# Kernel tuning notes

Hardware: AMD Instinct MI355X
Metric: run time of the kernel (lower is better)

## Reference

```python
import jax, jax.numpy as jnp
import numpy as np

BATCH = 512
SEQ = 500          # number of time points; SEQ-1 spline pieces
INPUT_CH = 8       # input (control) channels
HIDDEN = 64        # hidden channels (size of z)
HH = 128           # hidden_hidden channels of the CDE func MLP
OUT = 1            # output channels


def setup_inputs() -> dict:
    key = jax.random.key(0)
    ks = jax.random.split(key, 12)
    shp = (BATCH, SEQ - 1, INPUT_CH)
    times = jnp.linspace(0.0, 1.0, SEQ, dtype=jnp.float32)
    coeff_a = jax.random.normal(ks[0], shp, dtype=jnp.float32)
    coeff_b = jax.random.normal(ks[1], shp, dtype=jnp.float32)
    coeff_two_c = jax.random.normal(ks[2], shp, dtype=jnp.float32)
    coeff_three_d = jax.random.normal(ks[3], shp, dtype=jnp.float32)
    # learned parameters
    init_W = jax.random.normal(ks[4], (INPUT_CH, HIDDEN), dtype=jnp.float32) / np.sqrt(INPUT_CH)
    init_b = jnp.zeros((HIDDEN,), dtype=jnp.float32)
    f_W1 = jax.random.normal(ks[5], (HIDDEN, HH), dtype=jnp.float32) / np.sqrt(HIDDEN)
    f_b1 = jnp.zeros((HH,), dtype=jnp.float32)
    f_W2 = jax.random.normal(ks[6], (HH, HIDDEN * INPUT_CH), dtype=jnp.float32) / np.sqrt(HH)
    f_b2 = jnp.zeros((HIDDEN * INPUT_CH,), dtype=jnp.float32)
    lin_W = jax.random.normal(ks[7], (HIDDEN, OUT), dtype=jnp.float32) / np.sqrt(HIDDEN)
    lin_b = jnp.zeros((OUT,), dtype=jnp.float32)
    return dict(times=times, coeff_a=coeff_a, coeff_b=coeff_b,
                coeff_two_c=coeff_two_c, coeff_three_d=coeff_three_d,
                init_W=init_W, init_b=init_b, f_W1=f_W1, f_b1=f_b1,
                f_W2=f_W2, f_b2=f_b2, lin_W=lin_W, lin_b=lin_b)


def reference(times, coeff_a, coeff_b, coeff_two_c, coeff_three_d,
              init_W, init_b, f_W1, f_b1, f_W2, f_b2, lin_W, lin_b):
    n_pieces = coeff_b.shape[1]

    def _interpret_t(t):
        idx = jnp.clip(jnp.sum(t > times) - 1, 0, n_pieces - 1)
        frac = t - times[idx]
        return frac, idx

    def spline_eval(t):  # NaturalCubicSpline.evaluate -> (B, INPUT_CH)
        frac, idx = _interpret_t(t)
        inner = 0.5 * coeff_two_c[:, idx] + coeff_three_d[:, idx] * frac / 3.0
        inner = coeff_b[:, idx] + inner * frac
        return coeff_a[:, idx] + inner * frac

    def dX_dt(t):  # NaturalCubicSpline.derivative -> (B, INPUT_CH)
        frac, idx = _interpret_t(t)
        inner = coeff_two_c[:, idx] + coeff_three_d[:, idx] * frac
        return coeff_b[:, idx] + inner * frac

    def f(z):  # CDE vector field MLP -> (B, HIDDEN, INPUT_CH)
        h = jax.nn.relu(z @ f_W1 + f_b1)
        v = jnp.tanh(h @ f_W2 + f_b2)
        return v.reshape(z.shape[0], HIDDEN, INPUT_CH)

    def F(t, z):  # VectorField: f(z) @ dX/dt -> (B, HIDDEN)
        return jnp.einsum('bhi,bi->bh', f(z), dX_dt(t))

    # initial state from initial_network applied to X(t0)
    z0 = spline_eval(times[0]) @ init_W + init_b  # (B, HIDDEN)

    @jax.checkpoint
    def rk4_step(z, i):
        t0 = times[i]
        h = times[i + 1] - times[i]
        k1 = F(t0, z)
        k2 = F(t0 + 0.5 * h, z + 0.5 * h * k1)
        k3 = F(t0 + 0.5 * h, z + 0.5 * h * k2)
        k4 = F(t0 + h, z + h * k3)
        z_next = z + (h / 6.0) * (k1 + 2.0 * k2 + 2.0 * k3 + k4)
        return z_next, None

    zT, _ = jax.lax.scan(rk4_step, z0, jnp.arange(SEQ - 1))
    # final linear readout + sigmoid activation
    return jax.nn.sigmoid(zT @ lin_W + lin_b)  # (B, OUT)
```

## Files before the change

### kernel.cpp

```cpp
#include <hip/hip_runtime.h>
#include <hip/hip_bf16.h>

#define NPIECE 499

typedef __attribute__((ext_vector_type(8))) short bf16x8;
typedef __attribute__((ext_vector_type(4))) short s16x4;
typedef __attribute__((ext_vector_type(4))) float f32x4;

__device__ inline short f2bf(float x) {
    union { float f; unsigned u; } v; v.f = x;
    unsigned r = v.u + 0x7FFFu + ((v.u >> 16) & 1u);
    return (short)(r >> 16);
}

__device__ inline float fast_tanh(float x) {
    float e = __expf(2.0f * x);
    return 1.0f - 2.0f * __builtin_amdgcn_rcpf(e + 1.0f);
}

__global__ void __launch_bounds__(512, 2)
cde_kernel(const float* __restrict__ times,
           const float* __restrict__ ca,  const float* __restrict__ cb,
           const float* __restrict__ c2c, const float* __restrict__ c3d,
           const float* __restrict__ initW, const float* __restrict__ initb,
           const float* __restrict__ W1,  const float* __restrict__ b1,
           const float* __restrict__ W2,  const float* __restrict__ b2,
           const float* __restrict__ linW, const float* __restrict__ linb,
           float* __restrict__ out)
{
    const int tid  = threadIdx.x;
    const int lane = tid & 63;
    const int wv   = tid >> 6;
    const int g    = lane >> 4;
    const int col  = lane & 15;
    const int s0   = blockIdx.x * 2;

    __shared__ __align__(16) short hbuf[4][64][8];
    __shared__ __align__(16) short zbuf[2][64][8];
    __shared__ __align__(16) float vbuf[2][512];
    __shared__ __align__(16) float zcur[2][64];
    __shared__ __align__(16) float dxbuf[2][3][2][8];

    bf16x8 a2[4][4];
    float  binit2[4][4];
#pragma unroll
    for (int ot = 0; ot < 4; ++ot) {
        int o = 64 * wv + 16 * ot + col;
#pragma unroll
        for (int kk = 0; kk < 4; ++kk) {
            bf16x8 f;
#pragma unroll
            for (int e = 0; e < 8; ++e)
                f[e] = f2bf(W2[(32 * kk + 8 * g + e) * 512 + o]);
            a2[ot][kk] = f;
        }
#pragma unroll
        for (int r = 0; r < 4; ++r)
            binit2[ot][r] = b2[64 * wv + 16 * ot + 4 * g + r];
    }
    bf16x8 a1[2];
#pragma unroll
    for (int kk = 0; kk < 2; ++kk) {
        bf16x8 f;
#pragma unroll
        for (int e = 0; e < 8; ++e)
            f[e] = f2bf(W1[(32 * kk + 8 * g + e) * 128 + 16 * wv + col]);
        a1[kk] = f;
    }
    float binit1[4];
#pragma unroll
    for (int r = 0; r < 4; ++r) binit1[r] = b1[16 * wv + 4 * g + r];

    if (tid < 128) {
        int s = tid >> 6, hid = tid & 63;
        float z = initb[hid];
#pragma unroll
        for (int c = 0; c < 8; ++c)
            z += ca[((s0 + s) * NPIECE + 0) * 8 + c] * initW[c * 64 + hid];
        zcur[s][hid] = z;
        int ksub = hid >> 5, kin = hid & 31;
        zbuf[ksub][((kin >> 3) << 4) | s][kin & 7] = f2bf(z);
    }
    __syncthreads();

    float zreg = 0.f, zsreg = 0.f;
    {
        int m = lane & 31, s = lane >> 5;
        if ((m & 3) == 0) zreg = zcur[s][8 * wv + (m >> 2)];
    }

    for (int i = 0; i < NPIECE; ++i) {
        const float t0 = times[i];
        const float t1 = times[i + 1];
        const float h  = t1 - t0;
        const int par  = i & 1;

        if (tid < 16) {
            int s = tid >> 3, c = tid & 7;
            int rowbase = (s0 + s) * NPIECE * 8;
            int p0 = (i > 0) ? i - 1 : 0;
            float f0 = t0 - times[p0];
            int b0 = rowbase + p0 * 8 + c;
            dxbuf[par][0][s][c] = cb[b0] + (c2c[b0] + c3d[b0] * f0) * f0;
            float th = t0 + 0.5f * h;
            float f1 = th - t0;
            int bi = rowbase + i * 8 + c;
            dxbuf[par][1][s][c] = cb[bi] + (c2c[bi] + c3d[bi] * f1) * f1;
            float t3 = t0 + h;
            int bx; float f2v;
            if (i < NPIECE - 1 && t3 > t1) { bx = rowbase + (i + 1) * 8 + c; f2v = t3 - t1; }
            else                            { bx = bi;                        f2v = t3 - t0; }
            dxbuf[par][2][s][c] = cb[bx] + (c2c[bx] + c3d[bx] * f2v) * f2v;
        }

#pragma unroll
        for (int st = 0; st < 4; ++st) {
            const int dsel = (st == 0) ? 0 : ((st == 3) ? 2 : 1);
            __syncthreads();

            bf16x8 bz0 = *(const bf16x8*)&zbuf[0][lane][0];
            bf16x8 bz1 = *(const bf16x8*)&zbuf[1][lane][0];
            f32x4 acc1 = {binit1[0], binit1[1], binit1[2], binit1[3]};
            acc1 = __builtin_amdgcn_mfma_f32_16x16x32_bf16(a1[0], bz0, acc1, 0, 0, 0);
            acc1 = __builtin_amdgcn_mfma_f32_16x16x32_bf16(a1[1], bz1, acc1, 0, 0, 0);
            if (col < 2) {
                int h0 = 16 * wv + 4 * g;
                int ksub = h0 >> 5, kin = h0 & 31;
                s16x4 t;
                t[0] = f2bf(fmaxf(acc1[0], 0.f));
                t[1] = f2bf(fmaxf(acc1[1], 0.f));
                t[2] = f2bf(fmaxf(acc1[2], 0.f));
                t[3] = f2bf(fmaxf(acc1[3], 0.f));
                *(s16x4*)&hbuf[ksub][((kin >> 3) << 4) | col][kin & 7] = t;
            }
            __syncthreads();

            bf16x8 bh0 = *(const bf16x8*)&hbuf[0][lane][0];
            bf16x8 bh1 = *(const bf16x8*)&hbuf[1][lane][0];
            bf16x8 bh2 = *(const bf16x8*)&hbuf[2][lane][0];
            bf16x8 bh3 = *(const bf16x8*)&hbuf[3][lane][0];
            f32x4 c0 = {binit2[0][0], binit2[0][1], binit2[0][2], binit2[0][3]};
            f32x4 c1 = {binit2[1][0], binit2[1][1], binit2[1][2], binit2[1][3]};
            f32x4 c2r = {binit2[2][0], binit2[2][1], binit2[2][2], binit2[2][3]};
            f32x4 c3r = {binit2[3][0], binit2[3][1], binit2[3][2], binit2[3][3]};
            c0  = __builtin_amdgcn_mfma_f32_16x16x32_bf16(a2[0][0], bh0, c0, 0, 0, 0);
            c1  = __builtin_amdgcn_mfma_f32_16x16x32_bf16(a2[1][0], bh0, c1, 0, 0, 0);
            c2r = __builtin_amdgcn_mfma_f32_16x16x32_bf16(a2[2][0], bh0, c2r, 0, 0, 0);
            c3r = __builtin_amdgcn_mfma_f32_16x16x32_bf16(a2[3][0], bh0, c3r, 0, 0, 0);
            c0  = __builtin_amdgcn_mfma_f32_16x16x32_bf16(a2[0][1], bh1, c0, 0, 0, 0);
            c1  = __builtin_amdgcn_mfma_f32_16x16x32_bf16(a2[1][1], bh1, c1, 0, 0, 0);
            c2r = __builtin_amdgcn_mfma_f32_16x16x32_bf16(a2[2][1], bh1, c2r, 0, 0, 0);
            c3r = __builtin_amdgcn_mfma_f32_16x16x32_bf16(a2[3][1], bh1, c3r, 0, 0, 0);
            c0  = __builtin_amdgcn_mfma_f32_16x16x32_bf16(a2[0][2], bh2, c0, 0, 0, 0);
            c1  = __builtin_amdgcn_mfma_f32_16x16x32_bf16(a2[1][2], bh2, c1, 0, 0, 0);
            c2r = __builtin_amdgcn_mfma_f32_16x16x32_bf16(a2[2][2], bh2, c2r, 0, 0, 0);
            c3r = __builtin_amdgcn_mfma_f32_16x16x32_bf16(a2[3][2], bh2, c3r, 0, 0, 0);
            c0  = __builtin_amdgcn_mfma_f32_16x16x32_bf16(a2[0][3], bh3, c0, 0, 0, 0);
            c1  = __builtin_amdgcn_mfma_f32_16x16x32_bf16(a2[1][3], bh3, c1, 0, 0, 0);
            c2r = __builtin_amdgcn_mfma_f32_16x16x32_bf16(a2[2][3], bh3, c2r, 0, 0, 0);
            c3r = __builtin_amdgcn_mfma_f32_16x16x32_bf16(a2[3][3], bh3, c3r, 0, 0, 0);

            if (col < 2) {
                *(f32x4*)&vbuf[col][64 * wv + 0  + 4 * g] = c0;
                *(f32x4*)&vbuf[col][64 * wv + 16 + 4 * g] = c1;
                *(f32x4*)&vbuf[col][64 * wv + 32 + 4 * g] = c2r;
                *(f32x4*)&vbuf[col][64 * wv + 48 + 4 * g] = c3r;
            }
            asm volatile("s_waitcnt lgkmcnt(0)" ::: "memory");
            __builtin_amdgcn_wave_barrier();

            {
                int m = lane & 31, s = lane >> 5;
                int o = 64 * wv + 2 * m;
                float2 vv = *(const float2*)&vbuf[s][o];
                float va = fast_tanh(vv.x);
                float vb = fast_tanh(vv.y);
                const float* dxp = &dxbuf[par][dsel][s][0];
                float d0 = dxp[(2 * m) & 7];
                float d1 = dxp[(2 * m + 1) & 7];
                float p = va * d0 + vb * d1;
                p += __shfl_xor(p, 1);
                p += __shfl_xor(p, 2);
                if ((m & 3) == 0) {
                    int hid = 8 * wv + (m >> 2);
                    float k = p;
                    float zst;
                    if (st == 0)      { zsreg = k;             zst = zreg + 0.5f * h * k; }
                    else if (st == 1) { zsreg += 2.f * k;      zst = zreg + 0.5f * h * k; }
                    else if (st == 2) { zsreg += 2.f * k;      zst = zreg + h * k; }
                    else              { zsreg += k;            zst = zreg + (h / 6.f) * zsreg;
                                        zreg = zst;            zcur[s][hid] = zst; }
                    int ksub = hid >> 5, kin = hid & 31;
                    zbuf[ksub][((kin >> 3) << 4) | s][kin & 7] = f2bf(zst);
                }
            }
        }
    }

    __syncthreads();
    if (tid < 2) {
        float acc = linb[0];
        for (int hd = 0; hd < 64; ++hd) acc += zcur[tid][hd] * linW[hd];
        out[s0 + tid] = 1.0f / (1.0f + __expf(-acc));
    }
}

extern "C" void kernel_launch(void* const* d_in, const int* in_sizes, int n_in,
                              void* d_out, int out_size, void* d_ws, size_t ws_size,
                              hipStream_t stream) {
    (void)in_sizes; (void)n_in; (void)d_ws; (void)ws_size; (void)out_size;
    const float* times = (const float*)d_in[0];
    const float* ca    = (const float*)d_in[1];
    const float* cb    = (const float*)d_in[2];
    const float* c2c   = (const float*)d_in[3];
    const float* c3d   = (const float*)d_in[4];
    const float* initW = (const float*)d_in[5];
    const float* initb = (const float*)d_in[6];
    const float* W1    = (const float*)d_in[7];
    const float* b1    = (const float*)d_in[8];
    const float* W2    = (const float*)d_in[9];
    const float* b2    = (const float*)d_in[10];
    const float* linW  = (const float*)d_in[11];
    const float* linb  = (const float*)d_in[12];
    cde_kernel<<<256, 512, 0, stream>>>(times, ca, cb, c2c, c3d, initW, initb,
                                        W1, b1, W2, b2, linW, linb, (float*)d_out);
}
```

Measured before the change: 1.808 ms.

## Process one sample per 256-thread block and prefetch spline derivatives ahead

Each block now handles a single batch sample with four waves instead of two samples with eight waves, so each wave holds twice as many W2 tiles in registers (8x4 bf16x8 fragments) and does twice the MFMA work per stage. The spline-derivative values for the next piece are loaded into registers early in the iteration and written to shared memory in the last stage, overlapping global latency with compute. Times and b2 are cached in shared memory, the bias is added after the MFMA, and the final readout uses a wave shuffle reduction. The risk is higher register pressure from the doubled weight fragments, and the MFMA B operand now carries only one useful column out of sixteen.

```diff
diff --git a/kernel.cpp b/kernel.cpp
--- a/kernel.cpp
+++ b/kernel.cpp
@@ -2,6 +2,7 @@
 #include <hip/hip_bf16.h>
 
 #define NPIECE 499
+#define SEQN 500
 
 typedef __attribute__((ext_vector_type(8))) short bf16x8;
 typedef __attribute__((ext_vector_type(4))) short s16x4;
@@ -18,7 +19,7 @@
     return 1.0f - 2.0f * __builtin_amdgcn_rcpf(e + 1.0f);
 }
 
-__global__ void __launch_bounds__(512, 2)
+__global__ void __launch_bounds__(256, 2)
 cde_kernel(const float* __restrict__ times,
            const float* __restrict__ ca,  const float* __restrict__ cb,
            const float* __restrict__ c2c, const float* __restrict__ c3d,
@@ -33,84 +34,96 @@
     const int wv   = tid >> 6;
     const int g    = lane >> 4;
     const int col  = lane & 15;
-    const int s0   = blockIdx.x * 2;
-
-    __shared__ __align__(16) short hbuf[4][64][8];
-    __shared__ __align__(16) short zbuf[2][64][8];
-    __shared__ __align__(16) float vbuf[2][512];
-    __shared__ __align__(16) float zcur[2][64];
-    __shared__ __align__(16) float dxbuf[2][3][2][8];
-
-    bf16x8 a2[4][4];
-    float  binit2[4][4];
-#pragma unroll
-    for (int ot = 0; ot < 4; ++ot) {
-        int o = 64 * wv + 16 * ot + col;
+    const int s    = blockIdx.x;
+
+    __shared__ __align__(16) float tl[SEQN];
+    __shared__ __align__(16) float b2l[512];
+    __shared__ __align__(16) float vbuf[4][128];
+    __shared__ __align__(16) short hflat[128];
+    __shared__ __align__(16) short zflat[64];
+    __shared__ __align__(16) float zcur[64];
+    __shared__ __align__(16) float dxb[2][3][8];
+
+    for (int j = tid; j < SEQN; j += 256) tl[j] = times[j];
+    for (int j = tid; j < 512; j += 256) b2l[j] = b2[j];
+
+    bf16x8 a2[8][4];
+#pragma unroll
+    for (int t = 0; t < 8; ++t) {
+        int o = 128 * wv + 16 * t + col;
 #pragma unroll
         for (int kk = 0; kk < 4; ++kk) {
             bf16x8 f;
 #pragma unroll
             for (int e = 0; e < 8; ++e)
                 f[e] = f2bf(W2[(32 * kk + 8 * g + e) * 512 + o]);
-            a2[ot][kk] = f;
+            a2[t][kk] = f;
+        }
+    }
+    bf16x8 a1[2][2];
+    float binit1[2][4];
+#pragma unroll
+    for (int t = 0; t < 2; ++t) {
+        int o = 32 * wv + 16 * t + col;
+#pragma unroll
+        for (int kk = 0; kk < 2; ++kk) {
+            bf16x8 f;
+#pragma unroll
+            for (int e = 0; e < 8; ++e)
+                f[e] = f2bf(W1[(32 * kk + 8 * g + e) * 128 + o]);
+            a1[t][kk] = f;
         }
 #pragma unroll
         for (int r = 0; r < 4; ++r)
-            binit2[ot][r] = b2[64 * wv + 16 * ot + 4 * g + r];
-    }
-    bf16x8 a1[2];
-#pragma unroll
-    for (int kk = 0; kk < 2; ++kk) {
-        bf16x8 f;
-#pragma unroll
-        for (int e = 0; e < 8; ++e)
-            f[e] = f2bf(W1[(32 * kk + 8 * g + e) * 128 + 16 * wv + col]);
-        a1[kk] = f;
-    }
-    float binit1[4];
-#pragma unroll
-    for (int r = 0; r < 4; ++r) binit1[r] = b1[16 * wv + 4 * g + r];
-
-    if (tid < 128) {
-        int s = tid >> 6, hid = tid & 63;
-        float z = initb[hid];
+            binit1[t][r] = b1[32 * wv + 16 * t + 4 * g + r];
+    }
+
+    const size_t rowbase = (size_t)s * NPIECE * 8;
+
+    __syncthreads();
+
+    if (tid < 64) {
+        float z = initb[tid];
 #pragma unroll
         for (int c = 0; c < 8; ++c)
-            z += ca[((s0 + s) * NPIECE + 0) * 8 + c] * initW[c * 64 + hid];
-        zcur[s][hid] = z;
-        int ksub = hid >> 5, kin = hid & 31;
-        zbuf[ksub][((kin >> 3) << 4) | s][kin & 7] = f2bf(z);
+            z += ca[rowbase + c] * initW[c * 64 + tid];
+        zcur[tid] = z;
+        zflat[tid] = f2bf(z);
+    }
+    const int pslot = tid >> 3, pch = tid & 7;
+    if (tid < 24) {
+        float t0n = tl[0], t1n = tl[1], hn = t1n - t0n;
+        int p; float fr;
+        if (pslot == 0)      { p = 0; fr = 0.0f; }
+        else if (pslot == 1) { float th = t0n + 0.5f * hn; p = 0; fr = th - t0n; }
+        else { float t3 = t0n + hn;
+               if (t3 > t1n) { p = 1; fr = t3 - t1n; } else { p = 0; fr = t3 - t0n; } }
+        size_t off = rowbase + (size_t)p * 8 + pch;
+        dxb[0][pslot][pch] = cb[off] + (c2c[off] + c3d[off] * fr) * fr;
     }
     __syncthreads();
 
     float zreg = 0.f, zsreg = 0.f;
-    {
-        int m = lane & 31, s = lane >> 5;
-        if ((m & 3) == 0) zreg = zcur[s][8 * wv + (m >> 2)];
-    }
+    if ((lane & 3) == 0) zreg = zcur[16 * wv + (lane >> 2)];
 
     for (int i = 0; i < NPIECE; ++i) {
-        const float t0 = times[i];
-        const float t1 = times[i + 1];
-        const float h  = t1 - t0;
-        const int par  = i & 1;
-
-        if (tid < 16) {
-            int s = tid >> 3, c = tid & 7;
-            int rowbase = (s0 + s) * NPIECE * 8;
-            int p0 = (i > 0) ? i - 1 : 0;
-            float f0 = t0 - times[p0];
-            int b0 = rowbase + p0 * 8 + c;
-            dxbuf[par][0][s][c] = cb[b0] + (c2c[b0] + c3d[b0] * f0) * f0;
-            float th = t0 + 0.5f * h;
-            float f1 = th - t0;
-            int bi = rowbase + i * 8 + c;
-            dxbuf[par][1][s][c] = cb[bi] + (c2c[bi] + c3d[bi] * f1) * f1;
-            float t3 = t0 + h;
-            int bx; float f2v;
-            if (i < NPIECE - 1 && t3 > t1) { bx = rowbase + (i + 1) * 8 + c; f2v = t3 - t1; }
-            else                            { bx = bi;                        f2v = t3 - t0; }
-            dxbuf[par][2][s][c] = cb[bx] + (c2c[bx] + c3d[bx] * f2v) * f2v;
+        const float t0s = tl[i];
+        const float hs  = tl[i + 1] - t0s;
+        const int par = i & 1;
+
+        float pb = 0.f, pc = 0.f, pd = 0.f, pfr = 0.f;
+        const bool pf = (i + 1 < NPIECE) && (tid < 24);
+        if (pf) {
+            int j = i + 1;
+            float t0n = tl[j], t1n = tl[j + 1], hn = t1n - t0n;
+            int p; float fr;
+            if (pslot == 0)      { p = j - 1; fr = t0n - tl[j - 1]; }
+            else if (pslot == 1) { float th = t0n + 0.5f * hn; p = j; fr = th - t0n; }
+            else { float t3 = t0n + hn;
+                   if (j < NPIECE - 1 && t3 > t1n) { p = j + 1; fr = t3 - t1n; }
+                   else                            { p = j;     fr = t3 - t0n; } }
+            size_t off = rowbase + (size_t)p * 8 + pch;
+            pb = cb[off]; pc = c2c[off]; pd = c3d[off]; pfr = fr;
         }
 
 #pragma unroll
@@ -118,90 +131,92 @@
             const int dsel = (st == 0) ? 0 : ((st == 3) ? 2 : 1);
             __syncthreads();
 
-            bf16x8 bz0 = *(const bf16x8*)&zbuf[0][lane][0];
-            bf16x8 bz1 = *(const bf16x8*)&zbuf[1][lane][0];
-            f32x4 acc1 = {binit1[0], binit1[1], binit1[2], binit1[3]};
-            acc1 = __builtin_amdgcn_mfma_f32_16x16x32_bf16(a1[0], bz0, acc1, 0, 0, 0);
-            acc1 = __builtin_amdgcn_mfma_f32_16x16x32_bf16(a1[1], bz1, acc1, 0, 0, 0);
-            if (col < 2) {
-                int h0 = 16 * wv + 4 * g;
-                int ksub = h0 >> 5, kin = h0 & 31;
-                s16x4 t;
-                t[0] = f2bf(fmaxf(acc1[0], 0.f));
-                t[1] = f2bf(fmaxf(acc1[1], 0.f));
-                t[2] = f2bf(fmaxf(acc1[2], 0.f));
-                t[3] = f2bf(fmaxf(acc1[3], 0.f));
-                *(s16x4*)&hbuf[ksub][((kin >> 3) << 4) | col][kin & 7] = t;
+            if (st == 3 && pf)
+                dxb[par ^ 1][pslot][pch] = pb + (pc + pd * pfr) * pfr;
+
+            bf16x8 bz0 = *(const bf16x8*)&zflat[8 * g];
+            bf16x8 bz1 = *(const bf16x8*)&zflat[32 + 8 * g];
+            f32x4 h0 = {binit1[0][0], binit1[0][1], binit1[0][2], binit1[0][3]};
+            f32x4 h1 = {binit1[1][0], binit1[1][1], binit1[1][2], binit1[1][3]};
+            h0 = __builtin_amdgcn_mfma_f32_16x16x32_bf16(a1[0][0], bz0, h0, 0, 0, 0);
+            h1 = __builtin_amdgcn_mfma_f32_16x16x32_bf16(a1[1][0], bz0, h1, 0, 0, 0);
+            h0 = __builtin_amdgcn_mfma_f32_16x16x32_bf16(a1[0][1], bz1, h0, 0, 0, 0);
+            h1 = __builtin_amdgcn_mfma_f32_16x16x32_bf16(a1[1][1], bz1, h1, 0, 0, 0);
+            if (col == 0) {
+                s16x4 w0, w1;
+#pragma unroll
+                for (int r = 0; r < 4; ++r) {
+                    w0[r] = f2bf(fmaxf(h0[r], 0.f));
+                    w1[r] = f2bf(fmaxf(h1[r], 0.f));
+                }
+                *(s16x4*)&hflat[32 * wv + 4 * g]      = w0;
+                *(s16x4*)&hflat[32 * wv + 16 + 4 * g] = w1;
             }
             __syncthreads();
 
-            bf16x8 bh0 = *(const bf16x8*)&hbuf[0][lane][0];
-            bf16x8 bh1 = *(const bf16x8*)&hbuf[1][lane][0];
-            bf16x8 bh2 = *(const bf16x8*)&hbuf[2][lane][0];
-            bf16x8 bh3 = *(const bf16x8*)&hbuf[3][lane][0];
-            f32x4 c0 = {binit2[0][0], binit2[0][1], binit2[0][2], binit2[0][3]};
-            f32x4 c1 = {binit2[1][0], binit2[1][1], binit2[1][2], binit2[1][3]};
-            f32x4 c2r = {binit2[2][0], binit2[2][1], binit2[2][2], binit2[2][3]};
-            f32x4 c3r = {binit2[3][0], binit2[3][1], binit2[3][2], binit2[3][3]};
-            c0  = __builtin_amdgcn_mfma_f32_16x16x32_bf16(a2[0][0], bh0, c0, 0, 0, 0);
-            c1  = __builtin_amdgcn_mfma_f32_16x16x32_bf16(a2[1][0], bh0, c1, 0, 0, 0);
-            c2r = __builtin_amdgcn_mfma_f32_16x16x32_bf16(a2[2][0], bh0, c2r, 0, 0, 0);
-            c3r = __builtin_amdgcn_mfma_f32_16x16x32_bf16(a2[3][0], bh0, c3r, 0, 0, 0);
-            c0  = __builtin_amdgcn_mfma_f32_16x16x32_bf16(a2[0][1], bh1, c0, 0, 0, 0);
-            c1  = __builtin_amdgcn_mfma_f32_16x16x32_bf16(a2[1][1], bh1, c1, 0, 0, 0);
-            c2r = __builtin_amdgcn_mfma_f32_16x16x32_bf16(a2[2][1], bh1, c2r, 0, 0, 0);
-            c3r = __builtin_amdgcn_mfma_f32_16x16x32_bf16(a2[3][1], bh1, c3r, 0, 0, 0);
-            c0  = __builtin_amdgcn_mfma_f32_16x16x32_bf16(a2[0][2], bh2, c0, 0, 0, 0);
-            c1  = __builtin_amdgcn_mfma_f32_16x16x32_bf16(a2[1][2], bh2, c1, 0, 0, 0);
-            c2r = __builtin_amdgcn_mfma_f32_16x16x32_bf16(a2[2][2], bh2, c2r, 0, 0, 0);
-            c3r = __builtin_amdgcn_mfma_f32_16x16x32_bf16(a2[3][2], bh2, c3r, 0, 0, 0);
-            c0  = __builtin_amdgcn_mfma_f32_16x16x32_bf16(a2[0][3], bh3, c0, 0, 0, 0);
-            c1  = __builtin_amdgcn_mfma_f32_16x16x32_bf16(a2[1][3], bh3, c1, 0, 0, 0);
-            c2r = __builtin_amdgcn_mfma_f32_16x16x32_bf16(a2[2][3], bh3, c2r, 0, 0, 0);
-            c3r = __builtin_amdgcn_mfma_f32_16x16x32_bf16(a2[3][3], bh3, c3r, 0, 0, 0);
-
-            if (col < 2) {
-                *(f32x4*)&vbuf[col][64 * wv + 0  + 4 * g] = c0;
-                *(f32x4*)&vbuf[col][64 * wv + 16 + 4 * g] = c1;
-                *(f32x4*)&vbuf[col][64 * wv + 32 + 4 * g] = c2r;
-                *(f32x4*)&vbuf[col][64 * wv + 48 + 4 * g] = c3r;
+            bf16x8 bh0 = *(const bf16x8*)&hflat[8 * g];
+            bf16x8 bh1 = *(const bf16x8*)&hflat[32 + 8 * g];
+            bf16x8 bh2 = *(const bf16x8*)&hflat[64 + 8 * g];
+            bf16x8 bh3 = *(const bf16x8*)&hflat[96 + 8 * g];
+            f32x4 c[8];
+#pragma unroll
+            for (int t = 0; t < 8; ++t) c[t] = (f32x4){0.f, 0.f, 0.f, 0.f};
+#pragma unroll
+            for (int t = 0; t < 8; ++t)
+                c[t] = __builtin_amdgcn_mfma_f32_16x16x32_bf16(a2[t][0], bh0, c[t], 0, 0, 0);
+#pragma unroll
+            for (int t = 0; t < 8; ++t)
+                c[t] = __builtin_amdgcn_mfma_f32_16x16x32_bf16(a2[t][1], bh1, c[t], 0, 0, 0);
+#pragma unroll
+            for (int t = 0; t < 8; ++t)
+                c[t] = __builtin_amdgcn_mfma_f32_16x16x32_bf16(a2[t][2], bh2, c[t], 0, 0, 0);
+#pragma unroll
+            for (int t = 0; t < 8; ++t)
+                c[t] = __builtin_amdgcn_mfma_f32_16x16x32_bf16(a2[t][3], bh3, c[t], 0, 0, 0);
+
+            if (col == 0) {
+#pragma unroll
+                for (int t = 0; t < 8; ++t)
+                    *(f32x4*)&vbuf[wv][16 * t + 4 * g] = c[t];
             }
             asm volatile("s_waitcnt lgkmcnt(0)" ::: "memory");
             __builtin_amdgcn_wave_barrier();
 
             {
-                int m = lane & 31, s = lane >> 5;
-                int o = 64 * wv + 2 * m;
-                float2 vv = *(const float2*)&vbuf[s][o];
-                float va = fast_tanh(vv.x);
-                float vb = fast_tanh(vv.y);
-                const float* dxp = &dxbuf[par][dsel][s][0];
-                float d0 = dxp[(2 * m) & 7];
-                float d1 = dxp[(2 * m + 1) & 7];
-                float p = va * d0 + vb * d1;
+                float2 vv = *(const float2*)&vbuf[wv][2 * lane];
+                float2 bb = *(const float2*)&b2l[128 * wv + 2 * lane];
+                float va = fast_tanh(vv.x + bb.x);
+                float vb = fast_tanh(vv.y + bb.y);
+                float2 dd = *(const float2*)&dxb[par][dsel][(2 * lane) & 7];
+                float p = va * dd.x + vb * dd.y;
                 p += __shfl_xor(p, 1);
                 p += __shfl_xor(p, 2);
-                if ((m & 3) == 0) {
-                    int hid = 8 * wv + (m >> 2);
+                if ((lane & 3) == 0) {
+                    int hid = 16 * wv + (lane >> 2);
                     float k = p;
                     float zst;
-                    if (st == 0)      { zsreg = k;             zst = zreg + 0.5f * h * k; }
-                    else if (st == 1) { zsreg += 2.f * k;      zst = zreg + 0.5f * h * k; }
-                    else if (st == 2) { zsreg += 2.f * k;      zst = zreg + h * k; }
-                    else              { zsreg += k;            zst = zreg + (h / 6.f) * zsreg;
-                                        zreg = zst;            zcur[s][hid] = zst; }
-                    int ksub = hid >> 5, kin = hid & 31;
-                    zbuf[ksub][((kin >> 3) << 4) | s][kin & 7] = f2bf(zst);
+                    if (st == 0)      { zsreg = k;           zst = zreg + 0.5f * hs * k; }
+                    else if (st == 1) { zsreg += 2.f * k;    zst = zreg + 0.5f * hs * k; }
+                    else if (st == 2) { zsreg += 2.f * k;    zst = zreg + hs * k; }
+                    else              { zsreg += k;          zst = zreg + (hs / 6.f) * zsreg;
+                                        zreg = zst;          zcur[hid] = zst; }
+                    zflat[hid] = f2bf(zst);
                 }
             }
         }
     }
 
     __syncthreads();
-    if (tid < 2) {
-        float acc = linb[0];
-        for (int hd = 0; hd < 64; ++hd) acc += zcur[tid][hd] * linW[hd];
-        out[s0 + tid] = 1.0f / (1.0f + __expf(-acc));
+    if (wv == 0) {
+        float acc = zcur[lane] * linW[lane];
+        acc += __shfl_xor(acc, 1);
+        acc += __shfl_xor(acc, 2);
+        acc += __shfl_xor(acc, 4);
+        acc += __shfl_xor(acc, 8);
+        acc += __shfl_xor(acc, 16);
+        acc += __shfl_xor(acc, 32);
+        if (lane == 0)
+            out[s] = 1.0f / (1.0f + __expf(-(acc + linb[0])));
     }
 }
 
@@ -222,6 +237,6 @@
     const float* b2    = (const float*)d_in[10];
     const float* linW  = (const float*)d_in[11];
     const float* linb  = (const float*)d_in[12];
-    cde_kernel<<<256, 512, 0, stream>>>(times, ca, cb, c2c, c3d, initW, initb,
+    cde_kernel<<<512, 256, 0, stream>>>(times, ca, cb, c2c, c3d, initW, initb,
                                         W1, b1, W2, b2, linW, linb, (float*)d_out);
 }
```

Result: slower. 2.452 ms (+35.6%).
